# Kernel tuning notes

Hardware: AMD Instinct MI355X
Metric: run time of the kernel (lower is better)

The kernel has to match this reference:

```python
import math
import jax, jax.numpy as jnp
import numpy as np

BOHR2ANG = 0.52917721067
H2KJ = 2625.499638
RCUT = 10.0 / BOHR2ANG

# per-atom-type constants (type 0 = O, type 1 = H), atomic units
_Z    = np.array([3.61565, 0.93619])
_MONO = np.array([-0.390896, 0.195448])
_QSH  = _MONO - _Z
_DIPO = np.array([[0.0, 0.0, -0.094298], [0.0910288, 0.0, -0.207851]])
_QS   = np.array([[-0.330685, 0.0, 0.0, 0.869923, 0.0],
                  [-0.0739388, 0.0929482, 0.0, 0.00532425, 0.0]])
_B        = np.array([2.13358, 2.33322])
_B_PAULI  = np.array([2.1975, 1.96474])
_KM_PAULI = np.array([6.50923, 0.527804]) / _QSH
_KD_PAULI = np.array([-5.61925, -0.515584])
_KQ_PAULI = np.array([-1.56567, -0.440164])
_C6   = np.array([35.8289, 1.98954])
_B_D  = np.array([1.84302, 1.30993])
_ALPHA_M = np.stack([np.diag([4.45992, 6.07259, 4.55391]), np.diag([2.22001, 1.66835, 0.183855])])
_ETA  = np.array([6.18699e-06, 0.561535]) * 2.0
_B_XP = np.array([2.73582, 2.04028])
_KM_XP = np.array([1.26592, 0.200089]) / _QSH
_B_CT  = np.array([1.89485, 2.36763])
_KM_ACC = np.array([-0.67857, 1.36735]) / _QSH
_KM_DON = np.array([0.757752, 0.00888982]) / _QSH
_KD_DON = np.array([-0.512036, -0.0511668])
_KQ_DON = np.array([-0.208186, 0.0568152])
_EPS_OFF = 0.380979
_EPS_ON  = 1.0e15
_ZERO2 = np.zeros(2)

# bonded constants
_D_M   = 524.265 / H2KJ
_K_B   = 5098.15 / H2KJ * BOHR2ANG * BOHR2ANG
_B_EQ  = 0.958413 / BOHR2ANG
_K_BB  = -61.1423 / H2KJ * BOHR2ANG * BOHR2ANG
_K_BA  = -159.886 / H2KJ * BOHR2ANG
_TH_EQ = 104.4234 * math.pi / 180.0
_K_TH  = 452.183 / H2KJ
_BETA  = math.sqrt(_K_B / (2.0 * _D_M))

def _sph2cart(qs):
    # spherical [Q20,Q21c,Q21s,Q22c,Q22s] -> traceless Cartesian [T,3,3]
    s = math.sqrt(3.0) / 2.0
    q20, q21c, q21s, q22c, q22s = (qs[:, k] for k in range(5))
    qxx = -0.5 * q20 + s * q22c; qyy = -0.5 * q20 - s * q22c; qzz = q20
    qxy = s * q22s; qxz = s * q21c; qyz = s * q21s
    row = lambda a, b, c: np.stack([a, b, c], -1)
    return np.stack([row(qxx, qxy, qxz), row(qxy, qyy, qyz), row(qxz, qyz, qzz)], -2)

_QUAD = _sph2cart(_QS)

def _normalize(v):
    return v / jnp.linalg.norm(v, axis=-1, keepdims=True)

def _forward(coords, box, num_waters):
    W = int(num_waters); N = 3 * W
    dt = coords.dtype
    t = np.tile(np.array([0, 1, 1]), W)  # atom types
    g = lambda a: jnp.asarray(np.asarray(a, dtype=np.float64)[t], dtype=dt)

    # static index lists
    o = np.arange(W) * 3
    b0 = np.repeat(o, 2); b1 = b0 + np.tile(np.array([1, 2]), W)   # bonds O-H
    bb0 = np.arange(W) * 2; bb1 = bb0 + 1                          # two bonds per water
    ba_b = np.arange(2 * W); ba_a = np.repeat(np.arange(W), 2)
    idx = np.arange(N); m = idx % 3
    zat = np.where(m == 0, idx + 1, (idx // 3) * 3)
    xat = np.where(m == 0, idx + 2, np.where(m == 1, idx + 1, idx - 1))
    ax_bis = (m == 0)  # bisector frame on O
    ii, jj = np.divmod(np.arange(N * N), N)
    keep = (ii // 3) != (jj // 3)
    pi = ii[keep]; pj = jj[keep]  # ordered intermolecular pairs (both directions)

    boxinv = jnp.linalg.inv(box)
    def pbc(d):
        return d - jnp.round(d @ boxinv) @ box

    # ---- bonded terms ----
    bvec = pbc(coords[b1] - coords[b0])          # [2W,3] O->H
    blen = jnp.linalg.norm(bvec, axis=1)
    e_bond = jnp.sum(_D_M * (1.0 - jnp.exp(-_BETA * (blen - _B_EQ))) ** 2)
    e_bb = jnp.sum(_K_BB * (blen[bb0] - _B_EQ) * (blen[bb1] - _B_EQ))
    cosang = jnp.clip(jnp.sum(bvec[bb0] * bvec[bb1], 1) / (blen[bb0] * blen[bb1]), -1.0 + 1e-7, 1.0 - 1e-7)
    theta = jnp.arccos(cosang)
    e_ang = jnp.sum(0.5 * _K_TH * (cosang - math.cos(_TH_EQ)) ** 2)
    e_ba = jnp.sum(_K_BA * (blen[ba_b] - _B_EQ) * (theta[ba_a] - _TH_EQ))

    # ---- local->global frames, rotated multipoles ----
    uz = _normalize(pbc(coords[zat] - coords))
    ux = _normalize(pbc(coords[xat] - coords))
    zax = jnp.where(jnp.asarray(ax_bis)[:, None], _normalize(uz + ux), uz)
    xax = _normalize(ux - jnp.sum(ux * zax, 1, keepdims=True) * zax)
    yax = jnp.cross(zax, xax)
    R = jnp.stack([xax, yax, zax], axis=-1)      # [N,3,3] columns = local axes
    qsh = g(_QSH); Zc = g(_Z)
    mu = jnp.einsum('nab,nb->na', R, g(_DIPO))
    Qm = jnp.einsum('nab,nbc,ndc->nad', R, g(_QUAD), R) / 3.0   # 1/3 contraction weight
    alpha = jnp.einsum('nab,nbc,ndc->nad', R, g(_ALPHA_M), R)

    # ---- pairwise geometry ----
    dr = pbc(coords[pj] - coords[pi])
    r2 = jnp.sum(dr * dr, 1)
    r = jnp.sqrt(jnp.maximum(r2, 1e-12))
    w = (r < RCUT).astype(dt)
    n = dr / r[:, None]
    dot = lambda a: jnp.sum(a * n, 1)
    nQn = lambda Q: jnp.einsum('pa,pab,pb->p', n, Q, n)
    f1 = lambda u: 1.0 - jnp.exp(-u) * (1.0 + 0.5 * u)  # charge-penetration damping

    # ---- permanent electrostatics (core Z + damped shell multipoles) ----
    b_el = g(_B); bi, bj = b_el[pi], b_el[pj]
    fd = f1(jnp.sqrt(bi * bj) * r)
    qi, qj = qsh[pi], qsh[pj]; Zi, Zj = Zc[pi], Zc[pj]
    qti, qtj = Zi + qi, Zj + qj
    mui, muj = mu[pi], mu[pj]; muin, mujn = dot(mui), dot(muj)
    nQni, nQnj = nQn(Qm[pi]), nQn(Qm[pj])
    r3 = r * r2
    e_qq = (Zi * Zj + Zi * qj * f1(bj * r) + Zj * qi * f1(bi * r) + qi * qj * fd) / r
    e_qd = fd * (qtj * muin - qti * mujn) / r2
    e_dd = fd * (jnp.sum(mui * muj, 1) - 3.0 * muin * mujn) / r3
    e_qQ = 3.0 * fd * (qti * nQnj + qtj * nQni) / r3
    e_perm = 0.5 * jnp.sum(w * (e_qq + e_qd + e_dd + e_qQ))

    # ---- polarization: induced dipoles in the permanent field ----
    Ef_pair = (fd * w)[:, None] * (-(qtj / r2)[:, None] * n + (3.0 * mujn[:, None] * n - muj) / r3[:, None])
    Efld = jax.ops.segment_sum(Ef_pair, pi, num_segments=N)
    mu_ind = jnp.einsum('nab,nb->na', alpha, Efld)
    e_pol = -0.5 * jnp.sum(mu_ind * Efld)

    # ---- charge transfer (direct + indirect via transferred charge dq) ----
    q_acc = qsh * g(_KM_ACC); q_don = qsh * g(_KM_DON)
    mu_don = mu * g(_KD_DON)[:, None]; Q_don = Qm * g(_KQ_DON)[:, None, None]
    s_don_i = q_don[pi] + dot(mu_don[pi]) + nQn(Q_don[pi])
    s_don_j = q_don[pj] - dot(mu_don[pj]) + nQn(Q_don[pj])
    bct = g(_B_CT)
    Sct = jnp.exp(-jnp.sqrt(bct[pi] * bct[pj]) * r) * w
    e_ct_dir = -0.5 * jnp.sum((s_don_i * q_acc[pj] + s_don_j * q_acc[pi]) * Sct / r)
    eps_pair = jnp.asarray(np.where(t[pi] == t[pj], _EPS_ON, _EPS_OFF), dtype=dt)
    dq = jax.ops.segment_sum(s_don_i * q_acc[pj] * Sct / (eps_pair * r), pj, num_segments=N)
    e_ct_ind = 0.5 * jnp.sum(g(_ETA) * dq * dq)

    # ---- short-range overlap terms (Pauli repulsion, exchange polarization) ----
    def short_range(Km, Kd, Kq, b_arr, sign):
        qp = qsh * g(Km); mup = mu * g(Kd)[:, None]; Qp = Qm * g(Kq)[:, None, None]
        si = qp[pi] + dot(mup[pi]) + nQn(Qp[pi])
        sj = qp[pj] - dot(mup[pj]) + nQn(Qp[pj])
        bp = g(b_arr)
        return sign * 0.5 * jnp.sum(si * sj * jnp.exp(-jnp.sqrt(bp[pi] * bp[pj]) * r) / r * w)
    e_pauli = short_range(_KM_PAULI, _KD_PAULI, _KQ_PAULI, _B_PAULI, 1.0)
    e_xpol = short_range(_KM_XP, _ZERO2, _ZERO2, _B_XP, -1.0)

    # ---- Tang-Toennies damped dispersion ----
    bd = g(_B_D); c6 = g(_C6)
    u = jnp.sqrt(bd[pi] * bd[pj]) * r
    poly = sum(u ** k / math.factorial(k) for k in range(7))
    f6 = 1.0 - jnp.exp(-u) * poly
    e_disp = -0.5 * jnp.sum(w * f6 * jnp.sqrt(c6[pi] * c6[pj]) / (r2 * r2 * r2))

    return e_perm + e_pol + e_xpol + e_pauli + e_disp + e_ct_dir + e_ct_ind + e_bond + e_ang + e_bb + e_ba

NUM_WATERS = 256

def setup_inputs() -> dict:
    key = jax.random.key(0)
    W = NUM_WATERS
    side = 7
    spacing = 6.0  # bohr
    L = side * spacing
    grid = np.stack(np.meshgrid(*([np.arange(side)] * 3), indexing='ij'), -1).reshape(-1, 3)[:W] * spacing + 0.5 * spacing
    blen = 0.958413 / BOHR2ANG
    half = math.radians(104.4234 / 2.0)
    h1 = np.array([math.sin(half), 0.0, math.cos(half)]) * blen
    h2 = np.array([-math.sin(half), 0.0, math.cos(half)]) * blen
    coords = np.stack([grid, grid + h1, grid + h2], axis=1).reshape(-1, 3)
    coords = jnp.asarray(coords, dtype=jnp.float32) + 0.05 * jax.random.normal(key, (3 * W, 3), dtype=jnp.float32)
    box = jnp.eye(3, dtype=jnp.float32) * L
    return {"coords": coords, "box": box, "num_waters": W}

def reference(coords, box, num_waters):
    return _forward(coords, box, num_waters)
```

## Files before the change

kernel.cpp:

```cpp
#include <hip/hip_runtime.h>
#include <math.h>

constexpr double B2A   = 0.52917721067;
constexpr double H2KJ  = 2625.499638;
constexpr float  RCUT2F = (float)((10.0 / B2A) * (10.0 / B2A));

constexpr double Zc_[2]   = {3.61565, 0.93619};
constexpr double MONO_[2] = {-0.390896, 0.195448};
constexpr double QSH_[2]  = {MONO_[0] - Zc_[0], MONO_[1] - Zc_[1]};
constexpr double DIPO_[2][3] = {{0.0, 0.0, -0.094298},
                                {0.0910288, 0.0, -0.207851}};
constexpr double QS_[2][5] = {{-0.330685, 0.0, 0.0, 0.869923, 0.0},
                              {-0.0739388, 0.0929482, 0.0, 0.00532425, 0.0}};
constexpr double B_EL_[2]  = {2.13358, 2.33322};
constexpr double B_PA_[2]  = {2.1975, 1.96474};
constexpr double SPA_[2]   = {6.50923, 0.527804};
constexpr double KD_PA_[2] = {-5.61925, -0.515584};
constexpr double KQ_PA_[2] = {-1.56567, -0.440164};
constexpr double C6_[2]    = {35.8289, 1.98954};
constexpr double B_D_[2]   = {1.84302, 1.30993};
constexpr double AD_[2][3] = {{4.45992, 6.07259, 4.55391},
                              {2.22001, 1.66835, 0.183855}};
constexpr double ETA_[2]   = {6.18699e-06 * 2.0, 0.561535 * 2.0};
constexpr double B_XP_[2]  = {2.73582, 2.04028};
constexpr double SXP_[2]   = {1.26592, 0.200089};
constexpr double B_CT_[2]  = {1.89485, 2.36763};
constexpr double SACC_[2]  = {-0.67857, 1.36735};
constexpr double SDON_[2]  = {0.757752, 0.00888982};
constexpr double KD_DO_[2] = {-0.512036, -0.0511668};
constexpr double KQ_DO_[2] = {-0.208186, 0.0568152};
constexpr double EPS_OFF = 0.380979;

constexpr double D_M   = 524.265 / H2KJ;
constexpr double K_B   = 5098.15 / H2KJ * B2A * B2A;
constexpr double B_EQ  = 0.958413 / B2A;
constexpr double K_BB  = -61.1423 / H2KJ * B2A * B2A;
constexpr double K_BA  = -159.886 / H2KJ * B2A;
constexpr double TH_EQ = 104.4234 * M_PI / 180.0;
constexpr double K_TH  = 452.183 / H2KJ;
constexpr double SQ32  = 0.86602540378443864676;

constexpr double QLXX_[2] = {(-0.5 * QS_[0][0] + SQ32 * QS_[0][3]) / 3.0,
                             (-0.5 * QS_[1][0] + SQ32 * QS_[1][3]) / 3.0};
constexpr double QLYY_[2] = {(-0.5 * QS_[0][0] - SQ32 * QS_[0][3]) / 3.0,
                             (-0.5 * QS_[1][0] - SQ32 * QS_[1][3]) / 3.0};
constexpr double QLZZ_[2] = {QS_[0][0] / 3.0, QS_[1][0] / 3.0};
constexpr double QLXZ_[2] = {SQ32 * QS_[0][1] / 3.0, SQ32 * QS_[1][1] / 3.0};
constexpr double DIP0_[2] = {DIPO_[0][0], DIPO_[1][0]};
constexpr double DIP2_[2] = {DIPO_[0][2], DIPO_[1][2]};

#define MAXN 768
#define NWAVE 4
#define TF(A, t) ((t) ? (float)A[1] : (float)A[0])
#define S(x) (tb ? x##1 : x##0)

struct f3 { float x, y, z; };
__device__ inline f3 operator-(f3 a, f3 b) { return {a.x - b.x, a.y - b.y, a.z - b.z}; }
__device__ inline f3 operator+(f3 a, f3 b) { return {a.x + b.x, a.y + b.y, a.z + b.z}; }
__device__ inline f3 operator*(f3 a, float s) { return {a.x * s, a.y * s, a.z * s}; }
__device__ inline float dotf(f3 a, f3 b) { return a.x * b.x + a.y * b.y + a.z * b.z; }
__device__ inline f3 crossf(f3 a, f3 b) {
    return {a.y * b.z - a.z * b.y, a.z * b.x - a.x * b.z, a.x * b.y - a.y * b.x};
}
__device__ inline f3 normf(f3 a) { float s = rsqrtf(dotf(a, a)); return a * s; }
__device__ inline f3 getcf(const float* c, int i) {
    return {c[3 * i], c[3 * i + 1], c[3 * i + 2]};
}
__device__ inline void load_boxf(const float* box, float bx[3][3], float bi[3][3]) {
    for (int i = 0; i < 3; ++i)
        for (int j = 0; j < 3; ++j) bx[i][j] = box[i * 3 + j];
    float a = bx[0][0], b = bx[0][1], c = bx[0][2];
    float d = bx[1][0], e = bx[1][1], f = bx[1][2];
    float g = bx[2][0], h = bx[2][1], i2 = bx[2][2];
    float A =  (e * i2 - f * h), B = -(d * i2 - f * g), C =  (d * h - e * g);
    float D = -(b * i2 - c * h), E =  (a * i2 - c * g), F = -(a * h - b * g);
    float G =  (b * f - c * e),  H = -(a * f - c * d),  I =  (a * e - b * d);
    float s = 1.0f / (a * A + b * B + c * C);
    bi[0][0] = A * s; bi[0][1] = D * s; bi[0][2] = G * s;
    bi[1][0] = B * s; bi[1][1] = E * s; bi[1][2] = H * s;
    bi[2][0] = C * s; bi[2][1] = F * s; bi[2][2] = I * s;
}
__device__ inline f3 pbcf(f3 d, const float bx[3][3], const float bi[3][3]) {
    float s0 = rintf(d.x * bi[0][0] + d.y * bi[1][0] + d.z * bi[2][0]);
    float s1 = rintf(d.x * bi[0][1] + d.y * bi[1][1] + d.z * bi[2][1]);
    float s2 = rintf(d.x * bi[0][2] + d.y * bi[1][2] + d.z * bi[2][2]);
    d.x -= s0 * bx[0][0] + s1 * bx[1][0] + s2 * bx[2][0];
    d.y -= s0 * bx[0][1] + s1 * bx[1][1] + s2 * bx[2][1];
    d.z -= s0 * bx[0][2] + s1 * bx[1][2] + s2 * bx[2][2];
    return d;
}
__device__ inline float f1mf(float u) { return -__expf(-u) * (1.0f + 0.5f * u); }

struct d3 { double x, y, z; };
__device__ inline d3 subd(d3 a, d3 b) { return {a.x - b.x, a.y - b.y, a.z - b.z}; }
__device__ inline double dotd(d3 a, d3 b) { return a.x * b.x + a.y * b.y + a.z * b.z; }
__device__ inline d3 getcd(const float* c, int i) {
    return {(double)c[3 * i], (double)c[3 * i + 1], (double)c[3 * i + 2]};
}
__device__ inline void load_boxd(const float* box, double bx[3][3], double bi[3][3]) {
    for (int i = 0; i < 3; ++i)
        for (int j = 0; j < 3; ++j) bx[i][j] = (double)box[i * 3 + j];
    double a = bx[0][0], b = bx[0][1], c = bx[0][2];
    double d = bx[1][0], e = bx[1][1], f = bx[1][2];
    double g = bx[2][0], h = bx[2][1], i2 = bx[2][2];
    double A =  (e * i2 - f * h), B = -(d * i2 - f * g), C =  (d * h - e * g);
    double D = -(b * i2 - c * h), E =  (a * i2 - c * g), F = -(a * h - b * g);
    double G =  (b * f - c * e),  H = -(a * f - c * d),  I =  (a * e - b * d);
    double s = 1.0 / (a * A + b * B + c * C);
    bi[0][0] = A * s; bi[0][1] = D * s; bi[0][2] = G * s;
    bi[1][0] = B * s; bi[1][1] = E * s; bi[1][2] = H * s;
    bi[2][0] = C * s; bi[2][1] = F * s; bi[2][2] = I * s;
}
__device__ inline d3 pbcd(d3 d, const double bx[3][3], const double bi[3][3]) {
    double s0 = rint(d.x * bi[0][0] + d.y * bi[1][0] + d.z * bi[2][0]);
    double s1 = rint(d.x * bi[0][1] + d.y * bi[1][1] + d.z * bi[2][1]);
    double s2 = rint(d.x * bi[0][2] + d.y * bi[1][2] + d.z * bi[2][2]);
    d.x -= s0 * bx[0][0] + s1 * bx[1][0] + s2 * bx[2][0];
    d.y -= s0 * bx[0][1] + s1 * bx[1][1] + s2 * bx[2][1];
    d.z -= s0 * bx[0][2] + s1 * bx[1][2] + s2 * bx[2][2];
    return d;
}

__device__ inline void calc_frame(const float* coords, const float bx[3][3],
                                  const float bi[3][3], int n, float R[3][3], int* tt) {
    int w = n / 3, m = n - w * 3, o = w * 3;
    int zat = (m == 0) ? n + 1 : o;
    int xat = (m == 0) ? n + 2 : ((m == 1) ? n + 1 : n - 1);
    f3 cn = getcf(coords, n);
    f3 uz = normf(pbcf(getcf(coords, zat) - cn, bx, bi));
    f3 ux = normf(pbcf(getcf(coords, xat) - cn, bx, bi));
    f3 zax = (m == 0) ? normf(uz + ux) : uz;
    f3 xax = normf(ux - zax * dotf(ux, zax));
    f3 yax = crossf(zax, xax);
    R[0][0] = xax.x; R[0][1] = yax.x; R[0][2] = zax.x;
    R[1][0] = xax.y; R[1][1] = yax.y; R[1][2] = zax.y;
    R[2][0] = xax.z; R[2][1] = yax.z; R[2][2] = zax.z;
    *tt = (m == 0) ? 0 : 1;
}

__device__ inline void rot_muQ(const float R[3][3], int t, float M[9]) {
    float d0 = TF(DIP0_, t), d2 = TF(DIP2_, t);
    M[0] = R[0][0] * d0 + R[0][2] * d2;
    M[1] = R[1][0] * d0 + R[1][2] * d2;
    M[2] = R[2][0] * d0 + R[2][2] * d2;
    float qlxx = TF(QLXX_, t), qlyy = TF(QLYY_, t), qlzz = TF(QLZZ_, t), qlxz = TF(QLXZ_, t);
    float Bq[3][3];
    for (int p = 0; p < 3; ++p) {
        Bq[p][0] = R[p][0] * qlxx + R[p][2] * qlxz;
        Bq[p][1] = R[p][1] * qlyy;
        Bq[p][2] = R[p][0] * qlxz + R[p][2] * qlzz;
    }
    M[3] = Bq[0][0] * R[0][0] + Bq[0][1] * R[0][1] + Bq[0][2] * R[0][2];
    M[4] = Bq[0][0] * R[1][0] + Bq[0][1] * R[1][1] + Bq[0][2] * R[1][2];
    M[5] = Bq[0][0] * R[2][0] + Bq[0][1] * R[2][1] + Bq[0][2] * R[2][2];
    M[6] = Bq[1][0] * R[1][0] + Bq[1][1] * R[1][1] + Bq[1][2] * R[1][2];
    M[7] = Bq[1][0] * R[2][0] + Bq[1][1] * R[2][1] + Bq[1][2] * R[2][2];
    M[8] = Bq[2][0] * R[2][0] + Bq[2][1] * R[2][1] + Bq[2][2] * R[2][2];
}

__device__ inline float wredf(float v) {
    for (int off = 32; off > 0; off >>= 1) v += __shfl_xor(v, off);
    return v;
}
__device__ inline double wredd(double v) {
    for (int off = 32; off > 0; off >>= 1) v += __shfl_xor(v, off);
    return v;
}

__global__ void __launch_bounds__(256, 3)
k_main(const float* __restrict__ coords, const float* __restrict__ box,
       double* __restrict__ wsd, int N) {
    __shared__ float4 sh_list[MAXN];
    __shared__ float  sh_muQ[MAXN * 9];
    __shared__ double sh_red[NWAVE * 5];

    int a = blockIdx.x;
    int tid = threadIdx.x;
    int w = tid >> 6, lane = tid & 63;
    float bx[3][3], bi[3][3];
    load_boxf(box, bx, bi);

    int wa = a / 3;
    int ta = (a - wa * 3) ? 1 : 0;
    f3 ca = getcf(coords, a);

    float Ra[3][3]; int tt0;
    calc_frame(coords, bx, bi, a, Ra, &tt0);
    float MA[9];
    rot_muQ(Ra, ta, MA);
    f3 mua = {MA[0], MA[1], MA[2]};
    float Qaxx = MA[3], Qaxy = MA[4], Qaxz = MA[5], Qayy = MA[6], Qayz = MA[7], Qazz = MA[8];

    int chunks = (N + 64 * NWAVE - 1) / (64 * NWAVE);
    int seg = chunks * 64;
    int base = w * seg;
    int cnt = 0;
    for (int k = 0; k < chunks; ++k) {
        int b = base + k * 64 + lane;
        bool pred = false;
        f3 dr = {0.f, 0.f, 0.f};
        if (b < N) {
            int wb = b / 3;
            dr = pbcf(getcf(coords, b) - ca, bx, bi);
            pred = (wb != wa) && (dotf(dr, dr) < RCUT2F);
        }
        unsigned long long mask = __ballot(pred);
        int pref = __popcll(mask & ((1ull << lane) - 1ull));
        if (pred) sh_list[base + cnt + pref] = make_float4(dr.x, dr.y, dr.z, __int_as_float(b));
        cnt += __popcll(mask);
    }

    for (int i = lane; i < cnt; i += 64) {
        int b = __float_as_int(sh_list[base + i].w);
        float Rb[3][3]; int tb;
        calc_frame(coords, bx, bi, b, Rb, &tb);
        float MB[9];
        rot_muQ(Rb, tb, MB);
        float* dst = &sh_muQ[(base + i) * 9];
        for (int k = 0; k < 9; ++k) dst[k] = MB[k];
    }

    float Zi = TF(Zc_, ta), qi = TF(QSH_, ta), qti = Zi + qi;
    float beli = TF(B_EL_, ta);
    float belj0 = (float)B_EL_[0], belj1 = (float)B_EL_[1];
    float bije0 = sqrtf(beli * belj0), bije1 = sqrtf(beli * belj1);
    float qtj0 = (float)(Zc_[0] + QSH_[0]), qtj1 = (float)(Zc_[1] + QSH_[1]);
    float Ziqj0 = Zi * (float)QSH_[0], Ziqj1 = Zi * (float)QSH_[1];
    float Zjqi0 = (float)Zc_[0] * qi, Zjqi1 = (float)Zc_[1] * qi;
    float qiqj0 = qi * (float)QSH_[0], qiqj1 = qi * (float)QSH_[1];
    float qq0 = qti * qtj0, qq1 = qti * qtj1;
    float sacci = TF(SACC_, ta);
    float saccj0 = (float)SACC_[0], saccj1 = (float)SACC_[1];
    float sdi = TF(SDON_, ta), kddi = TF(KD_DO_, ta), kqdi = TF(KQ_DO_, ta);
    float sdj0 = (float)SDON_[0], sdj1 = (float)SDON_[1];
    float kddj0 = (float)KD_DO_[0], kddj1 = (float)KD_DO_[1];
    float kqdj0 = (float)KQ_DO_[0], kqdj1 = (float)KQ_DO_[1];
    float bctt = TF(B_CT_, ta);
    float bijct0 = sqrtf(bctt * (float)B_CT_[0]), bijct1 = sqrtf(bctt * (float)B_CT_[1]);
    float inve0 = (ta == 0) ? 1e-15f : (float)(1.0 / EPS_OFF);
    float inve1 = (ta == 1) ? 1e-15f : (float)(1.0 / EPS_OFF);
    float spi = TF(SPA_, ta), kdpi = TF(KD_PA_, ta), kqpi = TF(KQ_PA_, ta);
    float spj0 = (float)SPA_[0], spj1 = (float)SPA_[1];
    float kdpj0 = (float)KD_PA_[0], kdpj1 = (float)KD_PA_[1];
    float kqpj0 = (float)KQ_PA_[0], kqpj1 = (float)KQ_PA_[1];
    float bpat = TF(B_PA_, ta);
    float bijpa0 = sqrtf(bpat * (float)B_PA_[0]), bijpa1 = sqrtf(bpat * (float)B_PA_[1]);
    float bxpt = TF(B_XP_, ta);
    float bijxp0 = sqrtf(bxpt * (float)B_XP_[0]), bijxp1 = sqrtf(bxpt * (float)B_XP_[1]);
    float sxpi = TF(SXP_, ta);
    float cxp0 = sxpi * (float)SXP_[0], cxp1 = sxpi * (float)SXP_[1];
    float bdt = TF(B_D_, ta);
    float bijd0 = sqrtf(bdt * (float)B_D_[0]), bijd1 = sqrtf(bdt * (float)B_D_[1]);
    float c6t = TF(C6_, ta);
    float c60 = sqrtf(c6t * (float)C6_[0]), c61 = sqrtf(c6t * (float)C6_[1]);

    float e = 0.f, efx = 0.f, efy = 0.f, efz = 0.f, dqa = 0.f;
    for (int i = lane; i < cnt; i += 64) {
        float4 E4 = sh_list[base + i];
        f3 dr = {E4.x, E4.y, E4.z};
        int b = __float_as_int(E4.w);
        int wb = b / 3;
        int tb = (b - wb * 3) ? 1 : 0;
        float r2 = dotf(dr, dr);
        float invr = rsqrtf(r2);
        float r = r2 * invr;
        f3 nv = dr * invr;
        float invr2 = invr * invr, invr3 = invr2 * invr;

        const float* MB = &sh_muQ[(base + i) * 9];
        f3 mub = {MB[0], MB[1], MB[2]};
        float muin = dotf(mua, nv), mujn = dotf(mub, nv);
        float nQni = Qaxx * nv.x * nv.x + Qayy * nv.y * nv.y + Qazz * nv.z * nv.z +
                     2.f * (Qaxy * nv.x * nv.y + Qaxz * nv.x * nv.z + Qayz * nv.y * nv.z);
        float nQnj = MB[3] * nv.x * nv.x + MB[6] * nv.y * nv.y + MB[8] * nv.z * nv.z +
                     2.f * (MB[4] * nv.x * nv.y + MB[5] * nv.x * nv.z + MB[7] * nv.y * nv.z);

        float fdm = f1mf(S(bije) * r);
        float fd = 1.f + fdm;
        float ep = (S(qq) + S(Ziqj) * f1mf(S(belj) * r) + S(Zjqi) * f1mf(beli * r) +
                    S(qiqj) * fdm) * invr;
        ep += fd * (S(qtj) * muin - qti * mujn) * invr2;
        ep += fd * (dotf(mua, mub) - 3.f * muin * mujn) * invr3;
        ep += 3.f * fd * (qti * nQnj + S(qtj) * nQni) * invr3;

        float cc = -S(qtj) * invr2 + 3.f * mujn * invr3;
        efx += fd * (cc * nv.x - mub.x * invr3);
        efy += fd * (cc * nv.y - mub.y * invr3);
        efz += fd * (cc * nv.z - mub.z * invr3);

        float sdon_i = sdi + kddi * muin + kqdi * nQni;
        float sdon_j = S(sdj) - S(kddj) * mujn + S(kqdj) * nQnj;
        float sct_r = __expf(-S(bijct) * r) * invr;
        ep -= (sdon_i * S(saccj) + sdon_j * sacci) * sct_r;
        dqa += sdon_j * sacci * sct_r * S(inve);

        float si = spi + kdpi * muin + kqpi * nQni;
        float sj = S(spj) - S(kdpj) * mujn + S(kqpj) * nQnj;
        ep += si * sj * __expf(-S(bijpa) * r) * invr;

        ep -= S(cxp) * __expf(-S(bijxp) * r) * invr;

        float u = S(bijd) * r;
        float poly = 1.f + u * (1.f + u * (0.5f + u * (0.16666667f + u * (4.1666667e-2f +
                     u * (8.3333333e-3f + u * 1.3888889e-3f)))));
        ep -= (1.f - __expf(-u) * poly) * S(c6) * invr3 * invr3;

        e += ep;
    }

    e = wredf(e); efx = wredf(efx); efy = wredf(efy); efz = wredf(efz); dqa = wredf(dqa);
    if (lane == 0) {
        sh_red[w * 5 + 0] = (double)e;
        sh_red[w * 5 + 1] = (double)efx;
        sh_red[w * 5 + 2] = (double)efy;
        sh_red[w * 5 + 3] = (double)efz;
        sh_red[w * 5 + 4] = (double)dqa;
    }
    __syncthreads();

    if (tid == 0) {
        double se = 0, sx = 0, sy = 0, sz = 0, sq = 0;
        for (int k = 0; k < NWAVE; ++k) {
            se += sh_red[k * 5 + 0];
            sx += sh_red[k * 5 + 1];
            sy += sh_red[k * 5 + 2];
            sz += sh_red[k * 5 + 3];
            sq += sh_red[k * 5 + 4];
        }
        double tot = 0.5 * se;
        double v0 = (double)Ra[0][0] * sx + (double)Ra[1][0] * sy + (double)Ra[2][0] * sz;
        double v1 = (double)Ra[0][1] * sx + (double)Ra[1][1] * sy + (double)Ra[2][1] * sz;
        double v2 = (double)Ra[0][2] * sx + (double)Ra[1][2] * sy + (double)Ra[2][2] * sz;
        tot -= 0.5 * ((ta ? AD_[1][0] : AD_[0][0]) * v0 * v0 +
                      (ta ? AD_[1][1] : AD_[0][1]) * v1 * v1 +
                      (ta ? AD_[1][2] : AD_[0][2]) * v2 * v2);
        tot += 0.5 * (ta ? ETA_[1] : ETA_[0]) * sq * sq;

        if (ta == 0) {
            double bxd[3][3], bid[3][3];
            load_boxd(box, bxd, bid);
            d3 cO = getcd(coords, 3 * wa);
            d3 b1 = pbcd(subd(getcd(coords, 3 * wa + 1), cO), bxd, bid);
            d3 b2 = pbcd(subd(getcd(coords, 3 * wa + 2), cO), bxd, bid);
            double l1 = sqrt(dotd(b1, b1)), l2 = sqrt(dotd(b2, b2));
            double beta = sqrt(K_B / (2.0 * D_M));
            double x1 = 1.0 - exp(-beta * (l1 - B_EQ));
            double x2 = 1.0 - exp(-beta * (l2 - B_EQ));
            tot += D_M * (x1 * x1 + x2 * x2);
            tot += K_BB * (l1 - B_EQ) * (l2 - B_EQ);
            double cang = dotd(b1, b2) / (l1 * l2);
            cang = fmin(fmax(cang, -1.0 + 1e-7), 1.0 - 1e-7);
            double th = acos(cang);
            double cte = cos(TH_EQ);
            tot += 0.5 * K_TH * (cang - cte) * (cang - cte);
            tot += K_BA * ((l1 - B_EQ) + (l2 - B_EQ)) * (th - TH_EQ);
        }
        wsd[a] = tot;
    }
}

__global__ void __launch_bounds__(256) k_final(const double* __restrict__ wsd,
                                               float* __restrict__ out, int N) {
    int tid = threadIdx.x;
    int w = tid >> 6, lane = tid & 63;
    double v = 0.0;
    for (int i = tid; i < N; i += 256) v += wsd[i];
    v = wredd(v);
    __shared__ double s[4];
    if (lane == 0) s[w] = v;
    __syncthreads();
    if (tid == 0) out[0] = (float)(s[0] + s[1] + s[2] + s[3]);
}

extern "C" void kernel_launch(void* const* d_in, const int* in_sizes, int n_in,
                              void* d_out, int out_size, void* d_ws, size_t ws_size,
                              hipStream_t stream) {
    const float* coords = (const float*)d_in[0];
    const float* box    = (const float*)d_in[1];
    int N = in_sizes[0] / 3;
    double* wsd = (double*)d_ws;
    float* out = (float*)d_out;

    k_main<<<N, 256, 0, stream>>>(coords, box, wsd, N);
    k_final<<<1, 256, 0, stream>>>(wsd, out, N);
}
```

Before: 18.29 us.

## Split each atom's neighbor scan across two blocks and finalize nonlinear terms in reduction

Each atom is handled by two blocks of three waves, each half scanning interleaved 64-atom chunks, so twice as many smaller blocks run with less shared memory each. Partial energy, field and charge-transfer sums are written per half, and the quadratic polarization, charge-transfer and bonded terms are computed in the final single-block kernel after combining the halves. This raises occupancy and parallelism in the main kernel at the cost of duplicated per-atom frame setup and a heavier serial final kernel.

```diff
diff --git a/kernel.cpp b/kernel.cpp
--- a/kernel.cpp
+++ b/kernel.cpp
@@ -49,8 +49,8 @@
 constexpr double DIP0_[2] = {DIPO_[0][0], DIPO_[1][0]};
 constexpr double DIP2_[2] = {DIPO_[0][2], DIPO_[1][2]};
 
-#define MAXN 768
-#define NWAVE 4
+#define NWAVE 3
+#define SEG   128
 #define TF(A, t) ((t) ? (float)A[1] : (float)A[0])
 #define S(x) (tb ? x##1 : x##0)
 
@@ -162,19 +162,16 @@
     for (int off = 32; off > 0; off >>= 1) v += __shfl_xor(v, off);
     return v;
 }
-__device__ inline double wredd(double v) {
-    for (int off = 32; off > 0; off >>= 1) v += __shfl_xor(v, off);
-    return v;
-}
-
-__global__ void __launch_bounds__(256, 3)
+
+__global__ void __launch_bounds__(192, 4)
 k_main(const float* __restrict__ coords, const float* __restrict__ box,
        double* __restrict__ wsd, int N) {
-    __shared__ float4 sh_list[MAXN];
-    __shared__ float  sh_muQ[MAXN * 9];
+    __shared__ float4 sh_list[NWAVE * SEG];
+    __shared__ float  sh_muQ[NWAVE * SEG * 9];
     __shared__ double sh_red[NWAVE * 5];
 
-    int a = blockIdx.x;
+    int bid = blockIdx.x;
+    int a = bid >> 1, h = bid & 1;
     int tid = threadIdx.x;
     int w = tid >> 6, lane = tid & 63;
     float bx[3][3], bi[3][3];
@@ -191,12 +188,13 @@
     f3 mua = {MA[0], MA[1], MA[2]};
     float Qaxx = MA[3], Qaxy = MA[4], Qaxz = MA[5], Qayy = MA[6], Qayz = MA[7], Qazz = MA[8];
 
-    int chunks = (N + 64 * NWAVE - 1) / (64 * NWAVE);
-    int seg = chunks * 64;
-    int base = w * seg;
+    int nch = (N + 63) >> 6;
+    int base = w * SEG;
     int cnt = 0;
-    for (int k = 0; k < chunks; ++k) {
-        int b = base + k * 64 + lane;
+    for (int j = 2 * w; j <= 2 * w + 1; ++j) {
+        int c = h + 2 * j;
+        if (c >= nch) break;
+        int b = c * 64 + lane;
         bool pred = false;
         f3 dr = {0.f, 0.f, 0.f};
         if (b < N) {
@@ -327,49 +325,71 @@
             sz += sh_red[k * 5 + 3];
             sq += sh_red[k * 5 + 4];
         }
-        double tot = 0.5 * se;
-        double v0 = (double)Ra[0][0] * sx + (double)Ra[1][0] * sy + (double)Ra[2][0] * sz;
-        double v1 = (double)Ra[0][1] * sx + (double)Ra[1][1] * sy + (double)Ra[2][1] * sz;
-        double v2 = (double)Ra[0][2] * sx + (double)Ra[1][2] * sy + (double)Ra[2][2] * sz;
-        tot -= 0.5 * ((ta ? AD_[1][0] : AD_[0][0]) * v0 * v0 +
-                      (ta ? AD_[1][1] : AD_[0][1]) * v1 * v1 +
-                      (ta ? AD_[1][2] : AD_[0][2]) * v2 * v2);
-        tot += 0.5 * (ta ? ETA_[1] : ETA_[0]) * sq * sq;
-
-        if (ta == 0) {
-            double bxd[3][3], bid[3][3];
-            load_boxd(box, bxd, bid);
-            d3 cO = getcd(coords, 3 * wa);
-            d3 b1 = pbcd(subd(getcd(coords, 3 * wa + 1), cO), bxd, bid);
-            d3 b2 = pbcd(subd(getcd(coords, 3 * wa + 2), cO), bxd, bid);
+        wsd[bid] = 0.5 * se;
+        double* EF = wsd + 2 * N + bid * 3;
+        EF[0] = sx; EF[1] = sy; EF[2] = sz;
+        wsd[8 * N + bid] = sq;
+    }
+}
+
+__global__ void __launch_bounds__(256)
+k_final(const float* __restrict__ coords, const float* __restrict__ box,
+        const double* __restrict__ wsd, float* __restrict__ out, int N) {
+    int tid = threadIdx.x;
+    float bx[3][3], bi[3][3];
+    load_boxf(box, bx, bi);
+    double bxd[3][3], bid_[3][3];
+    load_boxd(box, bxd, bid_);
+
+    const double* EP = wsd;
+    const double* EF = wsd + 2 * N;
+    const double* DQ = wsd + 8 * N;
+
+    double e = 0.0;
+    for (int i = tid; i < N; i += 256) {
+        e += EP[2 * i] + EP[2 * i + 1];
+        double E0 = EF[(2 * i) * 3 + 0] + EF[(2 * i + 1) * 3 + 0];
+        double E1 = EF[(2 * i) * 3 + 1] + EF[(2 * i + 1) * 3 + 1];
+        double E2 = EF[(2 * i) * 3 + 2] + EF[(2 * i + 1) * 3 + 2];
+        float Ra[3][3]; int t;
+        calc_frame(coords, bx, bi, i, Ra, &t);
+        double v0 = (double)Ra[0][0] * E0 + (double)Ra[1][0] * E1 + (double)Ra[2][0] * E2;
+        double v1 = (double)Ra[0][1] * E0 + (double)Ra[1][1] * E1 + (double)Ra[2][1] * E2;
+        double v2 = (double)Ra[0][2] * E0 + (double)Ra[1][2] * E1 + (double)Ra[2][2] * E2;
+        e -= 0.5 * ((t ? AD_[1][0] : AD_[0][0]) * v0 * v0 +
+                    (t ? AD_[1][1] : AD_[0][1]) * v1 * v1 +
+                    (t ? AD_[1][2] : AD_[0][2]) * v2 * v2);
+        double dq = DQ[2 * i] + DQ[2 * i + 1];
+        e += 0.5 * (t ? ETA_[1] : ETA_[0]) * dq * dq;
+
+        if ((i % 3) == 0) {
+            int w = i / 3;
+            d3 cO = getcd(coords, 3 * w);
+            d3 b1 = pbcd(subd(getcd(coords, 3 * w + 1), cO), bxd, bid_);
+            d3 b2 = pbcd(subd(getcd(coords, 3 * w + 2), cO), bxd, bid_);
             double l1 = sqrt(dotd(b1, b1)), l2 = sqrt(dotd(b2, b2));
             double beta = sqrt(K_B / (2.0 * D_M));
             double x1 = 1.0 - exp(-beta * (l1 - B_EQ));
             double x2 = 1.0 - exp(-beta * (l2 - B_EQ));
-            tot += D_M * (x1 * x1 + x2 * x2);
-            tot += K_BB * (l1 - B_EQ) * (l2 - B_EQ);
+            e += D_M * (x1 * x1 + x2 * x2);
+            e += K_BB * (l1 - B_EQ) * (l2 - B_EQ);
             double cang = dotd(b1, b2) / (l1 * l2);
             cang = fmin(fmax(cang, -1.0 + 1e-7), 1.0 - 1e-7);
             double th = acos(cang);
             double cte = cos(TH_EQ);
-            tot += 0.5 * K_TH * (cang - cte) * (cang - cte);
-            tot += K_BA * ((l1 - B_EQ) + (l2 - B_EQ)) * (th - TH_EQ);
+            e += 0.5 * K_TH * (cang - cte) * (cang - cte);
+            e += K_BA * ((l1 - B_EQ) + (l2 - B_EQ)) * (th - TH_EQ);
         }
-        wsd[a] = tot;
-    }
-}
-
-__global__ void __launch_bounds__(256) k_final(const double* __restrict__ wsd,
-                                               float* __restrict__ out, int N) {
-    int tid = threadIdx.x;
-    int w = tid >> 6, lane = tid & 63;
-    double v = 0.0;
-    for (int i = tid; i < N; i += 256) v += wsd[i];
-    v = wredd(v);
-    __shared__ double s[4];
-    if (lane == 0) s[w] = v;
+    }
+
+    __shared__ double sh[256];
+    sh[tid] = e;
     __syncthreads();
-    if (tid == 0) out[0] = (float)(s[0] + s[1] + s[2] + s[3]);
+    for (int s = 128; s > 0; s >>= 1) {
+        if (tid < s) sh[tid] += sh[tid + s];
+        __syncthreads();
+    }
+    if (tid == 0) out[0] = (float)sh[0];
 }
 
 extern "C" void kernel_launch(void* const* d_in, const int* in_sizes, int n_in,
@@ -381,6 +401,6 @@
     double* wsd = (double*)d_ws;
     float* out = (float*)d_out;
 
-    k_main<<<N, 256, 0, stream>>>(coords, box, wsd, N);
-    k_final<<<1, 256, 0, stream>>>(wsd, out, N);
-}
+    k_main<<<2 * N, 192, 0, stream>>>(coords, box, wsd, N);
+    k_final<<<1, 256, 0, stream>>>(coords, box, wsd, out, N);
+}
```

Result: slower. 24.92 us (+36.2%).

## Fuse final reduction into main kernel using per-atom ready flags

Applied to the files above, without the earlier changes.

Removes the separate reduction kernel launch. Each block publishes its partial energy atomically with a per-atom flag. Block 0 spin-waits on all flags, sums the partials, resets the flags and writes the output. This saves one launch but risks deadlock if block 0 occupies a slot that blocks not yet scheduled need, and it relies on the workspace flags starting at zero on the first call.

```diff
diff --git a/kernel.cpp b/kernel.cpp
--- a/kernel.cpp
+++ b/kernel.cpp
@@ -51,6 +51,7 @@
 
 #define MAXN 768
 #define NWAVE 4
+#define MAGIC 0x5CA1AB1E
 #define TF(A, t) ((t) ? (float)A[1] : (float)A[0])
 #define S(x) (tb ? x##1 : x##0)
 
@@ -169,7 +170,8 @@
 
 __global__ void __launch_bounds__(256, 3)
 k_main(const float* __restrict__ coords, const float* __restrict__ box,
-       double* __restrict__ wsd, int N) {
+       double* __restrict__ wsd, int* __restrict__ flags,
+       float* __restrict__ out, int N) {
     __shared__ float4 sh_list[MAXN];
     __shared__ float  sh_muQ[MAXN * 9];
     __shared__ double sh_red[NWAVE * 5];
@@ -355,21 +357,27 @@
             tot += 0.5 * K_TH * (cang - cte) * (cang - cte);
             tot += K_BA * ((l1 - B_EQ) + (l2 - B_EQ)) * (th - TH_EQ);
         }
-        wsd[a] = tot;
-    }
-}
-
-__global__ void __launch_bounds__(256) k_final(const double* __restrict__ wsd,
-                                               float* __restrict__ out, int N) {
-    int tid = threadIdx.x;
-    int w = tid >> 6, lane = tid & 63;
-    double v = 0.0;
-    for (int i = tid; i < N; i += 256) v += wsd[i];
-    v = wredd(v);
-    __shared__ double s[4];
-    if (lane == 0) s[w] = v;
-    __syncthreads();
-    if (tid == 0) out[0] = (float)(s[0] + s[1] + s[2] + s[3]);
+        atomicExch((unsigned long long*)&wsd[a],
+                   (unsigned long long)__double_as_longlong(tot));
+        __threadfence();
+        atomicExch(&flags[a], MAGIC);
+    }
+
+    if (a == 0) {
+        __syncthreads();
+        double v = 0.0;
+        for (int i = tid; i < N; i += 256) {
+            while (atomicAdd(&flags[i], 0) != MAGIC) __builtin_amdgcn_s_sleep(2);
+            unsigned long long bits = atomicAdd((unsigned long long*)&wsd[i], 0ull);
+            v += __longlong_as_double((long long)bits);
+        }
+        v = wredd(v);
+        __shared__ double s2[4];
+        if (lane == 0) s2[w] = v;
+        __syncthreads();
+        for (int i = tid; i < N; i += 256) atomicExch(&flags[i], 0);
+        if (tid == 0) out[0] = (float)(s2[0] + s2[1] + s2[2] + s2[3]);
+    }
 }
 
 extern "C" void kernel_launch(void* const* d_in, const int* in_sizes, int n_in,
@@ -379,8 +387,8 @@
     const float* box    = (const float*)d_in[1];
     int N = in_sizes[0] / 3;
     double* wsd = (double*)d_ws;
+    int* flags = (int*)(wsd + N);
     float* out = (float*)d_out;
 
-    k_main<<<N, 256, 0, stream>>>(coords, box, wsd, N);
-    k_final<<<1, 256, 0, stream>>>(wsd, out, N);
-}
+    k_main<<<N, 256, 0, stream>>>(coords, box, wsd, flags, out, N);
+}
```

New measurement: 23.67 us. +29.4%, slower.
